# Optimization experiments

Measured on AMD Instinct MI355X. Metric: run time of the kernel, lower is better.

## Reference

```python
import jax, jax.numpy as jnp
import numpy as np

LEAK = 0.2
TEMP = 0.1          # CausalMask temperature
SPARSITY_W = 0.1
MI_W = 0.01
DAG_W = 1.0

def _leaky(x):
    return jax.nn.leaky_relu(x, LEAK)

def setup_inputs() -> dict:
    key = jax.random.key(0)
    B, F, S, H = 4096, 512, 32, 512
    H2, CH = H // 2, 64
    P = S * (S - 1) // 2  # 496 MI estimators
    ks = jax.random.split(key, 32)
    def w(k, shape, fan_in):
        return jax.random.normal(k, shape, jnp.float32) / np.sqrt(fan_in)
    return {
        'features': jax.random.normal(ks[0], (B, F), jnp.float32),
        'eps':      jax.random.normal(ks[1], (B, S), jnp.float32),
        'enc_w1': w(ks[2], (F, H), F),   'enc_b1': w(ks[3], (H,), H),
        'enc_w2': w(ks[4], (H, 2 * S), H), 'enc_b2': w(ks[5], (2 * S,), H) * 0.1,
        'log_weight': jax.random.normal(ks[6], (S, S), jnp.float32) * 0.5,
        'mech_w1': w(ks[7], (S, S, H2), S), 'mech_b1': w(ks[8], (S, H2), H2),
        'mech_w2': w(ks[9], (S, H2), H2),   'mech_b2': w(ks[10], (S,), H2),
        'dec_w1': w(ks[11], (S, H), S),  'dec_b1': w(ks[12], (H,), H),
        'dec_w2': w(ks[13], (H, F), H),  'dec_b2': w(ks[14], (F,), H),
        'mi_w1': w(ks[15], (P, 2, CH), 2),  'mi_b1': w(ks[16], (P, CH), CH),
        'mi_w2': w(ks[17], (P, CH, CH), CH), 'mi_b2': w(ks[18], (P, CH), CH),
        'mi_w3': w(ks[19], (P, CH), CH),     'mi_b3': w(ks[20], (P,), CH),
    }

def _forward(features, eps, enc_w1, enc_b1, enc_w2, enc_b2, log_weight,
             mech_w1, mech_b1, mech_w2, mech_b2, dec_w1, dec_b1, dec_w2, dec_b2,
             mi_w1, mi_b1, mi_w2, mi_b2, mi_w3, mi_b3):
    S = log_weight.shape[0]
    # ---- encode ----
    h = _leaky(features @ enc_w1 + enc_b1)
    params = h @ enc_w2 + enc_b2
    mean, log_std = jnp.split(params, 2, axis=-1)
    std = jnp.exp(log_std)
    z = mean + std * eps                                   # [B,S]
    # ---- soft causal adjacency (training mode) ----
    eye = jnp.eye(S, dtype=features.dtype)
    upper = jnp.triu(jnp.ones((S, S), features.dtype), k=1)
    lw = log_weight * upper - 10.0 * eye
    A = jax.nn.sigmoid(lw / TEMP)                          # [S,S]
    # ---- apply_causal_structure: stoch_dim tiny MLPs, vectorized ----
    # z_parents[b,i,s] = z[b,s] * A[s,i]
    zp = z[:, None, :] * A.T[None, :, :]                   # [B,S,S]
    h1 = _leaky(jnp.einsum('bis,ish->bih', zp, mech_w1) + mech_b1)  # [B,S,H2]
    z_causal = jnp.einsum('bih,ih->bi', h1, mech_w2) + mech_b2      # [B,S]
    # ---- decode ----
    recon = _leaky(z_causal @ dec_w1 + dec_b1) @ dec_w2 + dec_b2    # [B,F]
    # ---- losses ----
    recon_loss = jnp.mean((recon - features) ** 2)
    kl_loss = 0.5 * jnp.sum(mean ** 2 + std ** 2 - 2.0 * log_std - 1.0, axis=-1).mean()
    Asig = jax.nn.sigmoid(log_weight)
    sparsity_loss = jnp.sum(jnp.abs(Asig))
    # MI: one tiny MLP per (i<j) pair, row-major order == torch loop order
    iu, ju = jnp.triu_indices(S, k=1)
    pair = jnp.stack([z[:, iu], z[:, ju]], axis=-1)        # [B,P,2]
    m1 = _leaky(jnp.einsum('bpi,pih->bph', pair, mi_w1) + mi_b1)
    m2 = _leaky(jnp.einsum('bph,phk->bpk', m1, mi_w2) + mi_b2)
    mi_est = (jnp.einsum('bph,ph->bp', m2, mi_w3) + mi_b3).mean(0)  # [P]
    mi_loss = jnp.sum(jax.nn.sigmoid(log_weight[iu, ju]) * mi_est)
    # DAG: truncated matrix-exponential trace penalty
    A2 = Asig * Asig
    expm = eye
    mp = eye
    fact = 1.0
    for i in range(1, 10):
        fact *= i
        mp = mp @ A2
        expm = expm + mp / fact
    dag_loss = (jnp.trace(expm) - S) ** 2
    total_loss = recon_loss + kl_loss + SPARSITY_W * sparsity_loss + MI_W * mi_loss + DAG_W * dag_loss
    return z_causal, mean, std, recon, total_loss, recon_loss, kl_loss, sparsity_loss, mi_loss, dag_loss

def reference(features, eps, enc_w1, enc_b1, enc_w2, enc_b2, log_weight,
              mech_w1, mech_b1, mech_w2, mech_b2, dec_w1, dec_b1, dec_w2, dec_b2,
              mi_w1, mi_b1, mi_w2, mi_b2, mi_w3, mi_b3):
    return _forward(features, eps, enc_w1, enc_b1, enc_w2, enc_b2, log_weight,
                    mech_w1, mech_b1, mech_w2, mech_b2, dec_w1, dec_b1, dec_w2, dec_b2,
                    mi_w1, mi_b1, mi_w2, mi_b2, mi_w3, mi_b3)
```

## Files before the change

kernel.cpp:

```cpp
#include <hip/hip_runtime.h>
#include <hip/hip_bf16.h>

typedef float f32x4 __attribute__((ext_vector_type(4)));
typedef float f32x2 __attribute__((ext_vector_type(2)));
typedef short s16x8 __attribute__((ext_vector_type(8)));

__device__ __forceinline__ float leaky2(float x){ return fmaf(0.4f, fabsf(x), 0.6f * x); }

__device__ __forceinline__ short f2bf(float f){
    return __builtin_bit_cast(short, __float2bfloat16(f));
}

__global__ __launch_bounds__(256) void k_cvt(
    const float* __restrict__ feat, const float* __restrict__ ew1,
    const float* __restrict__ ew2, const float* __restrict__ dw2,
    const float* __restrict__ mw1, const float* __restrict__ mw2,
    const float* __restrict__ dw1,
    short* __restrict__ featbf, short* __restrict__ w1p,
    short* __restrict__ ew2p, short* __restrict__ dw2p,
    short* __restrict__ mw1p, short* __restrict__ mw2p,
    short* __restrict__ dw1p,
    const float* __restrict__ lw, float* __restrict__ A,
    float* __restrict__ acc)
{
    if (blockIdx.x >= 2048){
        __shared__ float A2s[1024], mp[1024], red[256];
        const int t = threadIdx.x;
        acc[t] = 0.f;
        acc[t + 256] = 0.f;
        float part = 0.f;
        #pragma unroll
        for (int q = 0; q < 4; ++q){
            int e = t * 4 + q;
            int r = e >> 5, c = e & 31;
            float v = lw[e];
            float sig = 1.f / (1.f + expf(-v));
            float l2 = (r < c) ? v * 10.f : ((r == c) ? -100.f : 0.f);
            A[e] = 1.f / (1.f + expf(-l2));
            part += sig;
            float a2 = sig * sig;
            A2s[e] = a2; mp[e] = a2;
        }
        red[t] = part; __syncthreads();
        for (int s = 128; s > 0; s >>= 1){ if (t < s) red[t] += red[t + s]; __syncthreads(); }
        if (t == 0) acc[2] = red[0];

        const float invf[10] = {0.f, 1.f, 0.5f, 1.6666667e-1f, 4.1666667e-2f,
                                8.3333333e-3f, 1.3888889e-3f, 1.9841270e-4f,
                                2.4801587e-5f, 2.7557319e-6f};
        float tr = 0.f;
        const int r = t >> 3, c0 = (t & 7) * 4;
        for (int n = 1; n <= 9; ++n){
            __syncthreads();
            if (t == 0){
                float s = 0.f;
                for (int k2 = 0; k2 < 32; ++k2) s += mp[k2 * 33];
                tr += s * invf[n];
            }
            if (n == 9) break;
            float av[4] = {0.f, 0.f, 0.f, 0.f};
            for (int k2 = 0; k2 < 32; ++k2){
                float m = mp[r * 32 + k2];
                #pragma unroll
                for (int q = 0; q < 4; ++q) av[q] = fmaf(m, A2s[k2 * 32 + c0 + q], av[q]);
            }
            __syncthreads();
            #pragma unroll
            for (int q = 0; q < 4; ++q) mp[r * 32 + c0 + q] = av[q];
        }
        if (t == 0) acc[3] = tr * tr;
        return;
    }
    for (int idx = blockIdx.x * 256 + threadIdx.x; idx < 620544; idx += 2048 * 256){
        int d = idx * 8;
        if (d < 2097152){
            f32x4 a0 = *(const f32x4*)&feat[d];
            f32x4 a1 = *(const f32x4*)&feat[d + 4];
            s16x8 v;
            #pragma unroll
            for (int e = 0; e < 4; ++e){ v[e] = f2bf(a0[e]); v[e + 4] = f2bf(a1[e]); }
            *(s16x8*)&featbf[d] = v;
            continue;
        }
        int s = d - 2097152;
        if (s < 262144){
            int t2 = s >> 9, lane = (s & 511) >> 3;
            int kb = (t2 & 15) * 32 + (lane >> 4) * 8;
            int n  = (t2 >> 4) * 16 + (lane & 15);
            s16x8 v;
            #pragma unroll
            for (int e = 0; e < 8; ++e) v[e] = f2bf(ew1[(kb + e) * 512 + n]);
            *(s16x8*)&w1p[s] = v;
            continue;
        }
        s -= 262144;
        if (s < 32768){
            int t2 = s >> 9, lane = (s & 511) >> 3;
            int kb = (t2 & 15) * 32 + (lane >> 4) * 8;
            int n  = (t2 >> 4) * 16 + (lane & 15);
            s16x8 v;
            #pragma unroll
            for (int e = 0; e < 8; ++e) v[e] = f2bf(ew2[(kb + e) * 64 + n]);
            *(s16x8*)&ew2p[s] = v;
            continue;
        }
        s -= 32768;
        if (s < 262144){
            int t2 = s >> 9, lane = (s & 511) >> 3;
            int kb = (t2 & 15) * 32 + (lane >> 4) * 8;
            int n  = (t2 >> 4) * 16 + (lane & 15);
            s16x8 v;
            #pragma unroll
            for (int e = 0; e < 8; ++e) v[e] = f2bf(dw2[(kb + e) * 512 + n]);
            *(s16x8*)&dw2p[s] = v;
            continue;
        }
        s -= 262144;
        if (s < 262144){
            int i = s >> 13, r2 = s & 8191;
            int nt = r2 >> 9, lane = (r2 & 511) >> 3;
            int kb = (lane >> 4) * 8;
            int n  = nt * 16 + (lane & 15);
            s16x8 v;
            #pragma unroll
            for (int e = 0; e < 8; ++e) v[e] = f2bf(mw1[i * 8192 + (kb + e) * 256 + n]);
            *(s16x8*)&mw1p[s + (i << 13) * 0] = v;
            continue;
        }
        s -= 262144;
        if (s < 2031616){
            int p = s >> 12, r2 = s & 4095;
            int tt = r2 >> 9, lane = (r2 & 511) >> 3;
            int nb = tt >> 1, ks = tt & 1;
            int kb = ks * 32 + (lane >> 4) * 8;
            int col = nb * 16 + (lane & 15);
            s16x8 v;
            #pragma unroll
            for (int e = 0; e < 8; ++e) v[e] = f2bf(mw2[(size_t)p * 4096 + (kb + e) * 64 + col]);
            *(s16x8*)&mw2p[s] = v;
            continue;
        }
        s -= 2031616;
        int nt = s >> 9, lane = (s & 511) >> 3;
        int kb = (lane >> 4) * 8;
        int n  = nt * 16 + (lane & 15);
        s16x8 v;
        #pragma unroll
        for (int e = 0; e < 8; ++e) v[e] = f2bf(dw1[(kb + e) * 512 + n]);
        *(s16x8*)&dw1p[s] = v;
    }
}

__global__ __launch_bounds__(256) void k_encf(
    const short* __restrict__ featbf, const short* __restrict__ w1p,
    const float* __restrict__ eb1, const short* __restrict__ ew2p,
    const float* __restrict__ eb2, const float* __restrict__ eps,
    float* __restrict__ omean, float* __restrict__ ostd,
    float* __restrict__ zt, float* __restrict__ accg)
{
    __shared__ short hlds[8192];
    __shared__ float P[16][65];
    __shared__ float zs[16][33];
    __shared__ float red[256];
    const int t = threadIdx.x, lane = t & 63, wv = t >> 6;
    const int ml = lane & 15, kg = lane >> 4;
    const int b0 = blockIdx.x * 16;

    f32x4 acc1[8] = {};
    for (int kt = 0; kt < 16; ++kt){
        s16x8 a = *(const s16x8*)&featbf[(size_t)(b0 + ml) * 512 + kt * 32 + kg * 8];
        #pragma unroll
        for (int nf = 0; nf < 8; ++nf){
            s16x8 b = *(const s16x8*)&w1p[((wv * 8 + nf) * 16 + kt) * 512 + lane * 8];
            acc1[nf] = __builtin_amdgcn_mfma_f32_16x16x32_bf16(a, b, acc1[nf], 0, 0, 0);
        }
    }
    #pragma unroll
    for (int nf = 0; nf < 8; ++nf){
        int col = wv * 128 + nf * 16 + ml;
        float bv = eb1[col];
        #pragma unroll
        for (int r = 0; r < 4; ++r){
            int row = kg * 4 + r;
            int byte = (row * 1024 + col * 2) ^ ((row & 7) << 4);
            hlds[byte >> 1] = f2bf(leaky2(acc1[nf][r] + bv));
        }
    }
    __syncthreads();

    f32x4 acc2 = {};
    for (int kt = 0; kt < 16; ++kt){
        int byte = (ml * 1024 + kt * 64 + kg * 16) ^ ((ml & 7) << 4);
        s16x8 a = *(const s16x8*)((const char*)hlds + byte);
        s16x8 b = *(const s16x8*)&ew2p[(wv * 16 + kt) * 512 + lane * 8];
        acc2 = __builtin_amdgcn_mfma_f32_16x16x32_bf16(a, b, acc2, 0, 0, 0);
    }
    {
        int col = wv * 16 + ml;
        float bv = eb2[col];
        #pragma unroll
        for (int r = 0; r < 4; ++r)
            P[kg * 4 + r][col] = acc2[r] + bv;
    }
    __syncthreads();
    float klp = 0.f;
    #pragma unroll
    for (int q = 0; q < 2; ++q){
        int e = q * 256 + t;
        int row = e >> 5, n = e & 31;
        float mean = P[row][n], ls = P[row][n + 32];
        float sd = expf(ls);
        size_t o = (size_t)(b0 + row) * 32 + n;
        float z = fmaf(sd, eps[o], mean);
        omean[o] = mean; ostd[o] = sd;
        zs[row][n] = z;
        klp += mean * mean + sd * sd - 2.f * ls - 1.f;
    }
    __syncthreads();
    #pragma unroll
    for (int q = 0; q < 2; ++q){
        int e = q * 256 + t;
        int n = e >> 4, row = e & 15;
        zt[(size_t)n * 4096 + b0 + row] = zs[row][n];
    }
    red[t] = klp; __syncthreads();
    for (int s = 128; s > 0; s >>= 1){ if (t < s) red[t] += red[t + s]; __syncthreads(); }
    if (t == 0) atomicAdd(accg + 0, red[0]);
}

__global__ __launch_bounds__(256) void k_mimech(
    const float* __restrict__ zt,
    const float* __restrict__ w1g, const float* __restrict__ b1g,
    const short* __restrict__ w2p, const float* __restrict__ b2g,
    const float* __restrict__ w3g, float* __restrict__ macc,
    const float* __restrict__ A, const short* __restrict__ W1p,
    const float* __restrict__ mb1, const float* __restrict__ mw2,
    const float* __restrict__ mb2, float* __restrict__ out_zc)
{
    __shared__ float sA[32], sB1[256], sW2[256];
    const int t = threadIdx.x, lane = t & 63, wv = t >> 6;
    const int ml = lane & 15, kg = lane >> 4;
    if (blockIdx.x < 1984){
        const int p = blockIdx.x >> 2, bq = blockIdx.x & 3;
        int pi = 0, rem = p;
        while (rem >= 31 - pi){ rem -= 31 - pi; ++pi; }
        const int pj = pi + 1 + rem;

        const int zrow = wv * 16 + ml;
        const float* zi_b = zt + (size_t)pi * 4096 + bq * 1024 + zrow;
        const float* zj_b = zt + (size_t)pj * 4096 + bq * 1024 + zrow;

        f32x2 w10v[2][4], w11v[2][4], b1v[2][4];
        #pragma unroll
        for (int ks = 0; ks < 2; ++ks)
            #pragma unroll
            for (int q = 0; q < 4; ++q){
                int h = ks * 32 + kg * 8 + q * 2;
                w10v[ks][q] = *(const f32x2*)&w1g[p * 128 + h] * 0.6f;
                w11v[ks][q] = *(const f32x2*)&w1g[p * 128 + 64 + h] * 0.6f;
                b1v[ks][q]  = *(const f32x2*)&b1g[p * 64 + h] * 0.6f;
            }
        s16x8 bfr[4][2];
        f32x4 b2c[4];
        #pragma unroll
        for (int nb = 0; nb < 4; ++nb){
            float bv = b2g[p * 64 + nb * 16 + ml];
            b2c[nb][0] = bv; b2c[nb][1] = bv; b2c[nb][2] = bv; b2c[nb][3] = bv;
            #pragma unroll
            for (int ks = 0; ks < 2; ++ks)
                bfr[nb][ks] = *(const s16x8*)&w2p[(size_t)p * 4096 + (nb * 2 + ks) * 512 + lane * 8];
        }
        const f32x2 c23 = {0.66666669f, 0.66666669f};
        float slin[4] = {0.f, 0.f, 0.f, 0.f}, sabs[4] = {0.f, 0.f, 0.f, 0.f};
        #pragma unroll 1
        for (int tile = 0; tile < 16; ++tile){
            float zi_c = zi_b[tile * 64], zj_c = zj_b[tile * 64];
            f32x2 zi2 = {zi_c, zi_c}, zj2 = {zj_c, zj_c};
            s16x8 af0, af1;
            #pragma unroll
            for (int q = 0; q < 4; ++q){
                f32x2 m0 = __builtin_elementwise_fma(zi2, w10v[0][q],
                           __builtin_elementwise_fma(zj2, w11v[0][q], b1v[0][q]));
                m0 = __builtin_elementwise_fma(c23, __builtin_elementwise_abs(m0), m0);
                af0[q * 2] = f2bf(m0[0]); af0[q * 2 + 1] = f2bf(m0[1]);
                f32x2 m1 = __builtin_elementwise_fma(zi2, w10v[1][q],
                           __builtin_elementwise_fma(zj2, w11v[1][q], b1v[1][q]));
                m1 = __builtin_elementwise_fma(c23, __builtin_elementwise_abs(m1), m1);
                af1[q * 2] = f2bf(m1[0]); af1[q * 2 + 1] = f2bf(m1[1]);
            }
            #pragma unroll
            for (int nb = 0; nb < 4; ++nb){
                f32x4 d = __builtin_amdgcn_mfma_f32_16x16x32_bf16(af0, bfr[nb][0], b2c[nb], 0, 0, 0);
                d = __builtin_amdgcn_mfma_f32_16x16x32_bf16(af1, bfr[nb][1], d, 0, 0, 0);
                #pragma unroll
                for (int r2 = 0; r2 < 4; ++r2){
                    slin[nb] += d[r2];
                    sabs[nb] += fabsf(d[r2]);
                }
            }
        }
        float s = 0.f;
        #pragma unroll
        for (int nb = 0; nb < 4; ++nb){
            float w3 = w3g[p * 64 + nb * 16 + ml];
            s = fmaf(0.6f * w3, slin[nb], fmaf(0.4f * w3, sabs[nb], s));
        }
        #pragma unroll
        for (int off = 32; off; off >>= 1) s += __shfl_xor(s, off);
        if (lane == 0) atomicAdd(&macc[p], s);
    } else {
        const int bx = blockIdx.x - 1984;
        const int i = bx & 31;
        const int b0 = (bx >> 5) * 64 + wv * 16;
        if (t < 32) sA[t] = A[t * 32 + i];
        sB1[t] = mb1[i * 256 + t];
        sW2[t] = mw2[i * 256 + t];
        __syncthreads();
        float zv[8];
        #pragma unroll
        for (int q = 0; q < 8; ++q)
            zv[q] = zt[(size_t)(kg * 8 + q) * 4096 + b0 + ml];
        s16x8 af;
        #pragma unroll
        for (int q = 0; q < 8; ++q)
            af[q] = f2bf(zv[q] * sA[kg * 8 + q]);
        float s[4] = {0.f, 0.f, 0.f, 0.f};
        #pragma unroll
        for (int nt = 0; nt < 16; ++nt){
            s16x8 bf = *(const s16x8*)&W1p[i * 8192 + nt * 512 + lane * 8];
            int col = nt * 16 + ml;
            float b1e = sB1[col], w2v = sW2[col];
            f32x4 d;
            d[0] = b1e; d[1] = b1e; d[2] = b1e; d[3] = b1e;
            d = __builtin_amdgcn_mfma_f32_16x16x32_bf16(af, bf, d, 0, 0, 0);
            float w2a = 0.6f * w2v, w2b = 0.4f * w2v;
            #pragma unroll
            for (int r = 0; r < 4; ++r)
                s[r] = fmaf(w2a, d[r], fmaf(w2b, fabsf(d[r]), s[r]));
        }
        #pragma unroll
        for (int off = 1; off < 16; off <<= 1)
            #pragma unroll
            for (int r = 0; r < 4; ++r) s[r] += __shfl_xor(s[r], off);
        if (ml == 0){
            float bb = mb2[i];
            #pragma unroll
            for (int r = 0; r < 4; ++r){
                int b = b0 + kg * 4 + r;
                out_zc[(size_t)b * 32 + i] = s[r] + bb;
            }
        }
    }
}

__global__ __launch_bounds__(256) void k_decf(
    const float* __restrict__ zc, const short* __restrict__ dw1p,
    const float* __restrict__ db1, const short* __restrict__ dw2p,
    const float* __restrict__ db2, const float* __restrict__ feat,
    float* __restrict__ recon, float* __restrict__ accg)
{
    __shared__ short dlds[16384];
    __shared__ float red[256];
    const int t = threadIdx.x, lane = t & 63, wv = t >> 6;
    const int ml = lane & 15, kg = lane >> 4;
    const int b0 = blockIdx.x * 32;
    const int c0 = blockIdx.y * 128;

    s16x8 af[2];
    #pragma unroll
    for (int m = 0; m < 2; ++m){
        int row = b0 + m * 16 + ml;
        f32x4 z0 = *(const f32x4*)&zc[(size_t)row * 32 + kg * 8];
        f32x4 z1 = *(const f32x4*)&zc[(size_t)row * 32 + kg * 8 + 4];
        #pragma unroll
        for (int e = 0; e < 4; ++e){
            af[m][e] = f2bf(z0[e]);
            af[m][e + 4] = f2bf(z1[e]);
        }
    }
    #pragma unroll
    for (int nf = 0; nf < 8; ++nf){
        int nt = wv * 8 + nf;
        s16x8 bf = *(const s16x8*)&dw1p[nt * 512 + lane * 8];
        int col = nt * 16 + ml;
        float b1e = db1[col];
        f32x4 c; c[0] = b1e; c[1] = b1e; c[2] = b1e; c[3] = b1e;
        #pragma unroll
        for (int m = 0; m < 2; ++m){
            f32x4 d = __builtin_amdgcn_mfma_f32_16x16x32_bf16(af[m], bf, c, 0, 0, 0);
            #pragma unroll
            for (int r = 0; r < 4; ++r){
                int row = m * 16 + kg * 4 + r;
                int byte = (row * 1024 + col * 2) ^ ((row & 7) << 4);
                dlds[byte >> 1] = f2bf(leaky2(d[r]));
            }
        }
    }
    __syncthreads();

    f32x4 acc[2][2] = {};
    for (int kt = 0; kt < 16; ++kt){
        s16x8 a[2];
        #pragma unroll
        for (int m = 0; m < 2; ++m){
            int row = m * 16 + ml;
            int byte = (row * 1024 + kt * 64 + kg * 16) ^ ((row & 7) << 4);
            a[m] = *(const s16x8*)((const char*)dlds + byte);
        }
        #pragma unroll
        for (int j = 0; j < 2; ++j){
            int nt = (c0 >> 4) + wv * 2 + j;
            s16x8 b = *(const s16x8*)&dw2p[(nt * 16 + kt) * 512 + lane * 8];
            #pragma unroll
            for (int m = 0; m < 2; ++m)
                acc[m][j] = __builtin_amdgcn_mfma_f32_16x16x32_bf16(a[m], b, acc[m][j], 0, 0, 0);
        }
    }
    float lsum = 0.f;
    #pragma unroll
    for (int j = 0; j < 2; ++j){
        int col = c0 + (wv * 2 + j) * 16 + ml;
        float bv = db2[col];
        #pragma unroll
        for (int m = 0; m < 2; ++m)
            #pragma unroll
            for (int r = 0; r < 4; ++r){
                int row = b0 + m * 16 + kg * 4 + r;
                float v = acc[m][j][r] + bv;
                float d = v - feat[(size_t)row * 512 + col];
                lsum = fmaf(d, d, lsum);
                recon[(size_t)row * 512 + col] = v;
            }
    }
    red[t] = lsum; __syncthreads();
    for (int s = 128; s > 0; s >>= 1){ if (t < s) red[t] += red[t + s]; __syncthreads(); }
    if (t == 0) atomicAdd(accg + 1, red[0]);
}

__global__ void k_final(const float* __restrict__ acc, const float* __restrict__ lw,
                        const float* __restrict__ b3, float* __restrict__ outs)
{
    __shared__ float red[512];
    int t = threadIdx.x;
    float c = 0.f;
    if (t < 496){
        int pi = 0, rem = t;
        while (rem >= 31 - pi){ rem -= 31 - pi; ++pi; }
        int pj = pi + 1 + rem;
        float est = acc[4 + t] * (1.f / 4096.f) + b3[t];
        float w = 1.f / (1.f + expf(-lw[pi * 32 + pj]));
        c = w * est;
    }
    red[t] = c; __syncthreads();
    for (int s = 256; s > 0; s >>= 1){ if (t < s) red[t] += red[t + s]; __syncthreads(); }
    if (t == 0){
        float mi    = red[0];
        float recon = acc[1] * (1.f / (4096.f * 512.f));
        float kl    = 0.5f * acc[0] * (1.f / 4096.f);
        float sp    = acc[2], dag = acc[3];
        outs[0] = recon + kl + 0.1f * sp + 0.01f * mi + dag;
        outs[1] = recon; outs[2] = kl; outs[3] = sp; outs[4] = mi; outs[5] = dag;
    }
}

extern "C" void kernel_launch(void* const* d_in, const int* in_sizes, int n_in,
                              void* d_out, int out_size, void* d_ws, size_t ws_size,
                              hipStream_t stream)
{
    const float* features = (const float*)d_in[0];
    const float* eps      = (const float*)d_in[1];
    const float* enc_w1   = (const float*)d_in[2];
    const float* enc_b1   = (const float*)d_in[3];
    const float* enc_w2   = (const float*)d_in[4];
    const float* enc_b2   = (const float*)d_in[5];
    const float* log_w    = (const float*)d_in[6];
    const float* mech_w1  = (const float*)d_in[7];
    const float* mech_b1  = (const float*)d_in[8];
    const float* mech_w2  = (const float*)d_in[9];
    const float* mech_b2  = (const float*)d_in[10];
    const float* dec_w1   = (const float*)d_in[11];
    const float* dec_b1   = (const float*)d_in[12];
    const float* dec_w2   = (const float*)d_in[13];
    const float* dec_b2   = (const float*)d_in[14];
    const float* mi_w1    = (const float*)d_in[15];
    const float* mi_b1    = (const float*)d_in[16];
    const float* mi_w2    = (const float*)d_in[17];
    const float* mi_b2    = (const float*)d_in[18];
    const float* mi_w3    = (const float*)d_in[19];
    const float* mi_b3    = (const float*)d_in[20];

    float* W      = (float*)d_ws;
    float* zt     = W;
    float* Abuf   = W + 262144;
    float* accums = W + 263168;
    short* w1p    = (short*)(W + 263680);
    short* ew2p   = (short*)(W + 394752);
    short* dw2p   = (short*)(W + 411136);
    short* mw1p   = (short*)(W + 542208);
    short* mw2p   = (short*)(W + 673280);
    short* dw1p   = (short*)(W + 1689088);
    float* out    = (float*)d_out;
    short* featbf = (short*)(out + 393216);

    k_cvt<<<2049, 256, 0, stream>>>(features, enc_w1, enc_w2, dec_w2, mech_w1, mi_w2,
                                    dec_w1, featbf, w1p, ew2p, dw2p, mw1p, mw2p, dw1p,
                                    log_w, Abuf, accums);
    k_encf<<<256, 256, 0, stream>>>(featbf, w1p, enc_b1, ew2p, enc_b2, eps,
                                    out + 131072, out + 262144, zt, accums);
    k_mimech<<<4032, 256, 0, stream>>>(zt, mi_w1, mi_b1, mw2p, mi_b2, mi_w3, accums + 4,
                                       Abuf, mw1p, mech_b1, mech_w2, mech_b2, out);
    k_decf<<<dim3(128, 4), 256, 0, stream>>>(out, dw1p, dec_b1, dw2p, dec_b2, features,
                                             out + 393216, accums);
    k_final<<<1, 512, 0, stream>>>(accums, log_w, mi_b3, out + 2490368);
}
```

Baseline: 121.8 us.

## Fuse decoder into MI/mechanism kernel with counter sync; widen encoder blocks

Merges the decoder kernel into the MI/mechanism kernel as trailing blocks that spin on a global counter until all 2048 mechanism blocks have written z_causal, so decoder work can overlap the MI tail and one launch disappears. The encoder kernel now uses 512 threads per block with half the N-fragments per wave, which raises parallelism per block. The spin-wait depends on the producer blocks being scheduled before the consumers, and the shared-memory footprint of every MI block grows. The cnt counter must be zeroed each call, which presumably happens in k_cvt.

```diff
diff --git a/kernel.cpp b/kernel.cpp
--- a/kernel.cpp
+++ b/kernel.cpp
@@ -124,7 +124,7 @@
             s16x8 v;
             #pragma unroll
             for (int e = 0; e < 8; ++e) v[e] = f2bf(mw1[i * 8192 + (kb + e) * 256 + n]);
-            *(s16x8*)&mw1p[s + (i << 13) * 0] = v;
+            *(s16x8*)&mw1p[s] = v;
             continue;
         }
         s -= 262144;
@@ -151,7 +151,7 @@
     }
 }
 
-__global__ __launch_bounds__(256) void k_encf(
+__global__ __launch_bounds__(512) void k_encf(
     const short* __restrict__ featbf, const short* __restrict__ w1p,
     const float* __restrict__ eb1, const short* __restrict__ ew2p,
     const float* __restrict__ eb2, const float* __restrict__ eps,
@@ -161,23 +161,23 @@
     __shared__ short hlds[8192];
     __shared__ float P[16][65];
     __shared__ float zs[16][33];
-    __shared__ float red[256];
+    __shared__ float red[512];
     const int t = threadIdx.x, lane = t & 63, wv = t >> 6;
     const int ml = lane & 15, kg = lane >> 4;
     const int b0 = blockIdx.x * 16;
 
-    f32x4 acc1[8] = {};
+    f32x4 acc1[4] = {};
     for (int kt = 0; kt < 16; ++kt){
         s16x8 a = *(const s16x8*)&featbf[(size_t)(b0 + ml) * 512 + kt * 32 + kg * 8];
         #pragma unroll
-        for (int nf = 0; nf < 8; ++nf){
-            s16x8 b = *(const s16x8*)&w1p[((wv * 8 + nf) * 16 + kt) * 512 + lane * 8];
+        for (int nf = 0; nf < 4; ++nf){
+            s16x8 b = *(const s16x8*)&w1p[((wv * 4 + nf) * 16 + kt) * 512 + lane * 8];
             acc1[nf] = __builtin_amdgcn_mfma_f32_16x16x32_bf16(a, b, acc1[nf], 0, 0, 0);
         }
     }
     #pragma unroll
-    for (int nf = 0; nf < 8; ++nf){
-        int col = wv * 128 + nf * 16 + ml;
+    for (int nf = 0; nf < 4; ++nf){
+        int col = wv * 64 + nf * 16 + ml;
         float bv = eb1[col];
         #pragma unroll
         for (int r = 0; r < 4; ++r){
@@ -188,14 +188,14 @@
     }
     __syncthreads();
 
-    f32x4 acc2 = {};
-    for (int kt = 0; kt < 16; ++kt){
-        int byte = (ml * 1024 + kt * 64 + kg * 16) ^ ((ml & 7) << 4);
-        s16x8 a = *(const s16x8*)((const char*)hlds + byte);
-        s16x8 b = *(const s16x8*)&ew2p[(wv * 16 + kt) * 512 + lane * 8];
-        acc2 = __builtin_amdgcn_mfma_f32_16x16x32_bf16(a, b, acc2, 0, 0, 0);
-    }
-    {
+    if (wv < 4){
+        f32x4 acc2 = {};
+        for (int kt = 0; kt < 16; ++kt){
+            int byte = (ml * 1024 + kt * 64 + kg * 16) ^ ((ml & 7) << 4);
+            s16x8 a = *(const s16x8*)((const char*)hlds + byte);
+            s16x8 b = *(const s16x8*)&ew2p[(wv * 16 + kt) * 512 + lane * 8];
+            acc2 = __builtin_amdgcn_mfma_f32_16x16x32_bf16(a, b, acc2, 0, 0, 0);
+        }
         int col = wv * 16 + ml;
         float bv = eb2[col];
         #pragma unroll
@@ -204,40 +204,41 @@
     }
     __syncthreads();
     float klp = 0.f;
-    #pragma unroll
-    for (int q = 0; q < 2; ++q){
-        int e = q * 256 + t;
-        int row = e >> 5, n = e & 31;
+    {
+        int row = t >> 5, n = t & 31;
         float mean = P[row][n], ls = P[row][n + 32];
         float sd = expf(ls);
         size_t o = (size_t)(b0 + row) * 32 + n;
         float z = fmaf(sd, eps[o], mean);
         omean[o] = mean; ostd[o] = sd;
         zs[row][n] = z;
-        klp += mean * mean + sd * sd - 2.f * ls - 1.f;
+        klp = mean * mean + sd * sd - 2.f * ls - 1.f;
     }
     __syncthreads();
-    #pragma unroll
-    for (int q = 0; q < 2; ++q){
-        int e = q * 256 + t;
-        int n = e >> 4, row = e & 15;
+    {
+        int n = t >> 4, row = t & 15;
         zt[(size_t)n * 4096 + b0 + row] = zs[row][n];
     }
     red[t] = klp; __syncthreads();
-    for (int s = 128; s > 0; s >>= 1){ if (t < s) red[t] += red[t + s]; __syncthreads(); }
+    for (int s = 256; s > 0; s >>= 1){ if (t < s) red[t] += red[t + s]; __syncthreads(); }
     if (t == 0) atomicAdd(accg + 0, red[0]);
 }
 
-__global__ __launch_bounds__(256) void k_mimech(
+__global__ __launch_bounds__(256) void k_mmd(
     const float* __restrict__ zt,
     const float* __restrict__ w1g, const float* __restrict__ b1g,
     const short* __restrict__ w2p, const float* __restrict__ b2g,
     const float* __restrict__ w3g, float* __restrict__ macc,
     const float* __restrict__ A, const short* __restrict__ W1p,
     const float* __restrict__ mb1, const float* __restrict__ mw2,
-    const float* __restrict__ mb2, float* __restrict__ out_zc)
+    const float* __restrict__ mb2, float* __restrict__ out_zc,
+    const short* __restrict__ dw1p, const float* __restrict__ db1,
+    const short* __restrict__ dw2p, const float* __restrict__ db2,
+    const float* __restrict__ feat, float* __restrict__ recon,
+    float* __restrict__ accg, int* __restrict__ cnt)
 {
-    __shared__ float sA[32], sB1[256], sW2[256];
+    __shared__ short dlds[16384];
+    __shared__ float red[256];
     const int t = threadIdx.x, lane = t & 63, wv = t >> 6;
     const int ml = lane & 15, kg = lane >> 4;
     if (blockIdx.x < 1984){
@@ -308,7 +309,10 @@
         #pragma unroll
         for (int off = 32; off; off >>= 1) s += __shfl_xor(s, off);
         if (lane == 0) atomicAdd(&macc[p], s);
-    } else {
+    } else if (blockIdx.x < 4032){
+        float* sA  = (float*)dlds;
+        float* sB1 = sA + 32;
+        float* sW2 = sB1 + 256;
         const int bx = blockIdx.x - 1984;
         const int i = bx & 31;
         const int b0 = (bx >> 5) * 64 + wv * 16;
@@ -350,91 +354,88 @@
                 out_zc[(size_t)b * 32 + i] = s[r] + bb;
             }
         }
-    }
-}
-
-__global__ __launch_bounds__(256) void k_decf(
-    const float* __restrict__ zc, const short* __restrict__ dw1p,
-    const float* __restrict__ db1, const short* __restrict__ dw2p,
-    const float* __restrict__ db2, const float* __restrict__ feat,
-    float* __restrict__ recon, float* __restrict__ accg)
-{
-    __shared__ short dlds[16384];
-    __shared__ float red[256];
-    const int t = threadIdx.x, lane = t & 63, wv = t >> 6;
-    const int ml = lane & 15, kg = lane >> 4;
-    const int b0 = blockIdx.x * 32;
-    const int c0 = blockIdx.y * 128;
-
-    s16x8 af[2];
-    #pragma unroll
-    for (int m = 0; m < 2; ++m){
-        int row = b0 + m * 16 + ml;
-        f32x4 z0 = *(const f32x4*)&zc[(size_t)row * 32 + kg * 8];
-        f32x4 z1 = *(const f32x4*)&zc[(size_t)row * 32 + kg * 8 + 4];
-        #pragma unroll
-        for (int e = 0; e < 4; ++e){
-            af[m][e] = f2bf(z0[e]);
-            af[m][e + 4] = f2bf(z1[e]);
-        }
-    }
-    #pragma unroll
-    for (int nf = 0; nf < 8; ++nf){
-        int nt = wv * 8 + nf;
-        s16x8 bf = *(const s16x8*)&dw1p[nt * 512 + lane * 8];
-        int col = nt * 16 + ml;
-        float b1e = db1[col];
-        f32x4 c; c[0] = b1e; c[1] = b1e; c[2] = b1e; c[3] = b1e;
+        __syncthreads();
+        if (t == 0){ __threadfence(); atomicAdd(cnt, 1); }
+    } else {
+        const int bx = blockIdx.x - 4032;
+        const int b0 = (bx >> 2) * 32;
+        const int c0 = (bx & 3) * 128;
+        if (t == 0){
+            while (atomicAdd(cnt, 0) < 2048) __builtin_amdgcn_s_sleep(32);
+            __threadfence();
+        }
+        __syncthreads();
+
+        s16x8 af[2];
         #pragma unroll
         for (int m = 0; m < 2; ++m){
-            f32x4 d = __builtin_amdgcn_mfma_f32_16x16x32_bf16(af[m], bf, c, 0, 0, 0);
-            #pragma unroll
-            for (int r = 0; r < 4; ++r){
-                int row = m * 16 + kg * 4 + r;
-                int byte = (row * 1024 + col * 2) ^ ((row & 7) << 4);
-                dlds[byte >> 1] = f2bf(leaky2(d[r]));
-            }
-        }
-    }
-    __syncthreads();
-
-    f32x4 acc[2][2] = {};
-    for (int kt = 0; kt < 16; ++kt){
-        s16x8 a[2];
-        #pragma unroll
-        for (int m = 0; m < 2; ++m){
-            int row = m * 16 + ml;
-            int byte = (row * 1024 + kt * 64 + kg * 16) ^ ((row & 7) << 4);
-            a[m] = *(const s16x8*)((const char*)dlds + byte);
-        }
+            int row = b0 + m * 16 + ml;
+            f32x4 z0 = *(const f32x4*)&out_zc[(size_t)row * 32 + kg * 8];
+            f32x4 z1 = *(const f32x4*)&out_zc[(size_t)row * 32 + kg * 8 + 4];
+            #pragma unroll
+            for (int e = 0; e < 4; ++e){
+                af[m][e] = f2bf(z0[e]);
+                af[m][e + 4] = f2bf(z1[e]);
+            }
+        }
+        #pragma unroll
+        for (int nf = 0; nf < 8; ++nf){
+            int nt = wv * 8 + nf;
+            s16x8 bf = *(const s16x8*)&dw1p[nt * 512 + lane * 8];
+            int col = nt * 16 + ml;
+            float b1e = db1[col];
+            f32x4 c; c[0] = b1e; c[1] = b1e; c[2] = b1e; c[3] = b1e;
+            #pragma unroll
+            for (int m = 0; m < 2; ++m){
+                f32x4 d = __builtin_amdgcn_mfma_f32_16x16x32_bf16(af[m], bf, c, 0, 0, 0);
+                #pragma unroll
+                for (int r = 0; r < 4; ++r){
+                    int row = m * 16 + kg * 4 + r;
+                    int byte = (row * 1024 + col * 2) ^ ((row & 7) << 4);
+                    dlds[byte >> 1] = f2bf(leaky2(d[r]));
+                }
+            }
+        }
+        __syncthreads();
+
+        f32x4 acc[2][2] = {};
+        for (int kt = 0; kt < 16; ++kt){
+            s16x8 a[2];
+            #pragma unroll
+            for (int m = 0; m < 2; ++m){
+                int row = m * 16 + ml;
+                int byte = (row * 1024 + kt * 64 + kg * 16) ^ ((row & 7) << 4);
+                a[m] = *(const s16x8*)((const char*)dlds + byte);
+            }
+            #pragma unroll
+            for (int j = 0; j < 2; ++j){
+                int nt = (c0 >> 4) + wv * 2 + j;
+                s16x8 b = *(const s16x8*)&dw2p[(nt * 16 + kt) * 512 + lane * 8];
+                #pragma unroll
+                for (int m = 0; m < 2; ++m)
+                    acc[m][j] = __builtin_amdgcn_mfma_f32_16x16x32_bf16(a[m], b, acc[m][j], 0, 0, 0);
+            }
+        }
+        float lsum = 0.f;
         #pragma unroll
         for (int j = 0; j < 2; ++j){
-            int nt = (c0 >> 4) + wv * 2 + j;
-            s16x8 b = *(const s16x8*)&dw2p[(nt * 16 + kt) * 512 + lane * 8];
+            int col = c0 + (wv * 2 + j) * 16 + ml;
+            float bv = db2[col];
             #pragma unroll
             for (int m = 0; m < 2; ++m)
-                acc[m][j] = __builtin_amdgcn_mfma_f32_16x16x32_bf16(a[m], b, acc[m][j], 0, 0, 0);
-        }
-    }
-    float lsum = 0.f;
-    #pragma unroll
-    for (int j = 0; j < 2; ++j){
-        int col = c0 + (wv * 2 + j) * 16 + ml;
-        float bv = db2[col];
-        #pragma unroll
-        for (int m = 0; m < 2; ++m)
-            #pragma unroll
-            for (int r = 0; r < 4; ++r){
-                int row = b0 + m * 16 + kg * 4 + r;
-                float v = acc[m][j][r] + bv;
-                float d = v - feat[(size_t)row * 512 + col];
-                lsum = fmaf(d, d, lsum);
-                recon[(size_t)row * 512 + col] = v;
-            }
-    }
-    red[t] = lsum; __syncthreads();
-    for (int s = 128; s > 0; s >>= 1){ if (t < s) red[t] += red[t + s]; __syncthreads(); }
-    if (t == 0) atomicAdd(accg + 1, red[0]);
+                #pragma unroll
+                for (int r = 0; r < 4; ++r){
+                    int row = b0 + m * 16 + kg * 4 + r;
+                    float v = acc[m][j][r] + bv;
+                    float d = v - feat[(size_t)row * 512 + col];
+                    lsum = fmaf(d, d, lsum);
+                    recon[(size_t)row * 512 + col] = v;
+                }
+        }
+        red[t] = lsum; __syncthreads();
+        for (int s = 128; s > 0; s >>= 1){ if (t < s) red[t] += red[t + s]; __syncthreads(); }
+        if (t == 0) atomicAdd(accg + 1, red[0]);
+    }
 }
 
 __global__ void k_final(const float* __restrict__ acc, const float* __restrict__ lw,
@@ -505,11 +506,11 @@
     k_cvt<<<2049, 256, 0, stream>>>(features, enc_w1, enc_w2, dec_w2, mech_w1, mi_w2,
                                     dec_w1, featbf, w1p, ew2p, dw2p, mw1p, mw2p, dw1p,
                                     log_w, Abuf, accums);
-    k_encf<<<256, 256, 0, stream>>>(featbf, w1p, enc_b1, ew2p, enc_b2, eps,
+    k_encf<<<256, 512, 0, stream>>>(featbf, w1p, enc_b1, ew2p, enc_b2, eps,
                                     out + 131072, out + 262144, zt, accums);
-    k_mimech<<<4032, 256, 0, stream>>>(zt, mi_w1, mi_b1, mw2p, mi_b2, mi_w3, accums + 4,
-                                       Abuf, mw1p, mech_b1, mech_w2, mech_b2, out);
-    k_decf<<<dim3(128, 4), 256, 0, stream>>>(out, dw1p, dec_b1, dw2p, dec_b2, features,
-                                             out + 393216, accums);
+    k_mmd<<<4544, 256, 0, stream>>>(zt, mi_w1, mi_b1, mw2p, mi_b2, mi_w3, accums + 4,
+                                    Abuf, mw1p, mech_b1, mech_w2, mech_b2, out,
+                                    dw1p, dec_b1, dw2p, dec_b2, features,
+                                    out + 393216, accums, (int*)(accums + 500));
     k_final<<<1, 512, 0, stream>>>(accums, log_w, mi_b3, out + 2490368);
 }
```

Measured after the change: 208.3 us. 70.9% more time.
